# Kernel tuning notes

Hardware: AMD Instinct MI355X
Metric: run time of the kernel (lower is better)

Reference implementation:

```python
import jax, jax.numpy as jnp
import numpy as np

B, T, D, HS = 32, 2048, 384, 64

def setup_inputs() -> dict:
    key = jax.random.key(0)
    kx, kq, kk, kv = jax.random.split(key, 4)
    x = jax.random.normal(kx, (B, T, D), dtype=jnp.float32)
    s = 1.0 / np.sqrt(D)  # Linear-like init scale
    Wq = jax.random.normal(kq, (D, HS), dtype=jnp.float32) * s
    Wk = jax.random.normal(kk, (D, HS), dtype=jnp.float32) * s
    Wv = jax.random.normal(kv, (D, HS), dtype=jnp.float32) * s
    return {"x": x, "Wq": Wq, "Wk": Wk, "Wv": Wv}

def reference(x, Wq, Wk, Wv):
    # Single-head causal self-attention (dropout in eval mode -> identity).
    Tlen = x.shape[1]
    q = x @ Wq  # [B,T,HS]
    k = x @ Wk
    v = x @ Wv
    scale = q.shape[-1] ** (-0.5)
    wei = jnp.einsum('bqd,bkd->bqk', q, k) * scale  # [B,T,T]
    causal = jnp.tril(jnp.ones((Tlen, Tlen), dtype=bool))
    wei = jnp.where(causal, wei, jnp.finfo(wei.dtype).min)
    wei = jax.nn.softmax(wei, axis=-1)
    return jnp.einsum('bqk,bkd->bqd', wei, v)  # [B,T,HS]
```

## Files before the change

### kernel.cpp

```cpp
#include <hip/hip_runtime.h>
#include <hip/hip_bf16.h>

#define T_LEN 2048
#define NBATCH 32

typedef __bf16 bf16x8 __attribute__((ext_vector_type(8)));
typedef float f32x4 __attribute__((ext_vector_type(4)));

__device__ __forceinline__ unsigned short f2bf(float f) {
  return __builtin_bit_cast(unsigned short, __float2bfloat16(f));
}
__device__ __forceinline__ unsigned int pk2(float a, float b) {
  return (unsigned int)f2bf(a) | ((unsigned int)f2bf(b) << 16);
}
__device__ __forceinline__ bf16x8 ld16(const void* p) {
  return __builtin_bit_cast(bf16x8, *(const uint4*)p);
}
__device__ __forceinline__ void gl_lds16(const void* g, void* l) {
  __builtin_amdgcn_global_load_lds(
      (const __attribute__((address_space(1))) unsigned int*)g,
      (__attribute__((address_space(3))) unsigned int*)l, 16, 0, 0);
}
__device__ __forceinline__ void bar_raw() {
  asm volatile("s_barrier" ::: "memory");
}

__global__ __launch_bounds__(256) void k_wprep(const float* __restrict__ Wq,
                                               const float* __restrict__ Wk,
                                               const float* __restrict__ Wv,
                                               unsigned short* __restrict__ Wt3) {
  int idx = blockIdx.x * 256 + threadIdx.x;
  if (idx >= 192 * 384) return;
  int c = idx / 384;
  int k = idx % 384;
  const float* W = (c < 64) ? Wq : ((c < 128) ? Wk : Wv);
  Wt3[idx] = f2bf(W[k * 64 + (c & 63)]);
}

__global__ __launch_bounds__(256) void k_proj(const float* __restrict__ x,
                                              const unsigned short* __restrict__ Wt3,
                                              unsigned short* __restrict__ Qb,
                                              unsigned short* __restrict__ Kb,
                                              unsigned short* __restrict__ VTb) {
  __shared__ __align__(16) unsigned short xs[128 * 32];
  __shared__ __align__(16) unsigned short wt[192 * 32];
  const int tid = threadIdx.x;
  const int lane = tid & 63, w = tid >> 6;
  const int g = lane >> 4, lr = lane & 15;
  const long row0 = (long)blockIdx.x * 128;

  f32x4 acc[2][12] = {};

  for (int ks = 0; ks < 12; ++ks) {
    const int k0 = ks * 32;
    __syncthreads();
    {
      int r = tid >> 1, c0 = (tid & 1) * 16;
      const float4* src = reinterpret_cast<const float4*>(&x[(row0 + r) * 384 + k0 + c0]);
      float4 f0 = src[0], f1 = src[1], f2 = src[2], f3 = src[3];
      uint4 u0, u1;
      u0.x = pk2(f0.x, f0.y); u0.y = pk2(f0.z, f0.w);
      u0.z = pk2(f1.x, f1.y); u0.w = pk2(f1.z, f1.w);
      u1.x = pk2(f2.x, f2.y); u1.y = pk2(f2.z, f2.w);
      u1.z = pk2(f3.x, f3.y); u1.w = pk2(f3.z, f3.w);
      int b0 = (r * 64 + c0 * 2) ^ ((r & 7) << 4);
      int b1 = (r * 64 + c0 * 2 + 16) ^ ((r & 7) << 4);
      *reinterpret_cast<uint4*>((char*)xs + b0) = u0;
      *reinterpret_cast<uint4*>((char*)xs + b1) = u1;
    }
#pragma unroll
    for (int j = 0; j < 3; ++j) {
      int chunk = tid + 256 * j;
      int r = chunk >> 2, c8 = chunk & 3;
      uint4 d = *reinterpret_cast<const uint4*>(&Wt3[r * 384 + k0 + c8 * 8]);
      int b = (r * 64 + c8 * 16) ^ ((r & 7) << 4);
      *reinterpret_cast<uint4*>((char*)wt + b) = d;
    }
    __syncthreads();

    bf16x8 a[2];
#pragma unroll
    for (int mt = 0; mt < 2; ++mt) {
      int r = w * 32 + mt * 16 + lr;
      a[mt] = ld16((char*)xs + ((r * 64 + g * 16) ^ ((r & 7) << 4)));
    }
#pragma unroll
    for (int n = 0; n < 12; ++n) {
      int r = n * 16 + lr;
      bf16x8 bb = ld16((char*)wt + ((r * 64 + g * 16) ^ ((r & 7) << 4)));
      acc[0][n] = __builtin_amdgcn_mfma_f32_16x16x32_bf16(a[0], bb, acc[0][n], 0, 0, 0);
      acc[1][n] = __builtin_amdgcn_mfma_f32_16x16x32_bf16(a[1], bb, acc[1][n], 0, 0, 0);
    }
  }

#pragma unroll
  for (int mt = 0; mt < 2; ++mt)
#pragma unroll
    for (int n = 0; n < 12; ++n)
#pragma unroll
      for (int rr = 0; rr < 4; ++rr) {
        long grow = row0 + w * 32 + mt * 16 + g * 4 + rr;
        int col = n * 16 + lr;
        unsigned short hv = f2bf(acc[mt][n][rr]);
        if (n < 4) {
          Qb[grow * 64 + col] = hv;
        } else if (n < 8) {
          Kb[grow * 64 + (col - 64)] = hv;
        } else {
          long bb_ = grow >> 11;
          long t = grow & 2047;
          VTb[(bb_ * 64 + (col - 128)) * 2048 + t] = hv;
        }
      }
}

__global__ __launch_bounds__(256, 4) void k_attn(const unsigned short* __restrict__ Qb,
                                                 const unsigned short* __restrict__ Kb,
                                                 const unsigned short* __restrict__ VTb,
                                                 float* __restrict__ out) {
  __shared__ __align__(16) char ksm[2 * 8192];
  __shared__ __align__(16) char vsm[2 * 8192];
  __shared__ __align__(16) unsigned short psm[4 * 16 * 64];

  const int tid = threadIdx.x;
  const int lane = tid & 63, w = tid >> 6;
  const int g = lane >> 4, lr = lane & 15;
  const int b = blockIdx.x;
  const int p = blockIdx.y;

  const char* Kg = (const char*)(Kb + (long)b * T_LEN * 64);
  const char* Vg = (const char*)(VTb + (long)b * 64 * 2048);

  const int lrow = lane >> 3;
  const int lsw = (((lane & 7) ^ lrow) << 4);

  const float C2 = 0.125f * 1.44269504f;
  char* pbase = (char*)psm + w * 2048;

  for (int phase = 0; phase < 2; ++phase) {
    const int qt = phase ? p : (31 - p);
    const int qrow0 = qt * 64 + w * 16;
    const int nkv = qt + 1;

    bf16x8 qf[2];
#pragma unroll
    for (int c = 0; c < 2; ++c)
      qf[c] = ld16(&Qb[((long)(b * T_LEN + qrow0 + lr)) * 64 + c * 32 + g * 8]);

    f32x4 o[4] = {};
    float m2[4], l_r[4];
#pragma unroll
    for (int r = 0; r < 4; ++r) { m2[r] = -1e30f; l_r[r] = 0.f; }

    {
      const char* gk = Kg + ((long)(w * 16 + lrow)) * 128 + lsw;
      const char* gv = Vg + ((long)(w * 16 + lrow)) * 4096 + lsw;
      char* kb = ksm + w * 2048;
      char* vb = vsm + w * 2048;
      gl_lds16(gk, kb);             gl_lds16(gk + 8 * 128, kb + 1024);
      gl_lds16(gv, vb);             gl_lds16(gv + 8 * 4096, vb + 1024);
    }

    int cur = 0;
    for (int t = 0; t < nkv; ++t) {
      const int kv0 = t * 64;

      bar_raw();

      if (t + 1 < nkv) {
        const int kv1 = kv0 + 64;
        const char* gk = Kg + ((long)(kv1 + w * 16 + lrow)) * 128 + lsw;
        const char* gv = Vg + ((long)(w * 16 + lrow)) * 4096 + (long)kv1 * 2 + lsw;
        char* kb = ksm + (cur ^ 1) * 8192 + w * 2048;
        char* vb = vsm + (cur ^ 1) * 8192 + w * 2048;
        gl_lds16(gk, kb);           gl_lds16(gk + 8 * 128, kb + 1024);
        gl_lds16(gv, vb);           gl_lds16(gv + 8 * 4096, vb + 1024);
        asm volatile("s_waitcnt vmcnt(4)" ::: "memory");
      } else {
        asm volatile("s_waitcnt vmcnt(0)" ::: "memory");
      }
      bar_raw();

      char* kt = ksm + cur * 8192;
      char* vt = vsm + cur * 8192;

      f32x4 s[4] = {};
      __builtin_amdgcn_s_setprio(1);
#pragma unroll
      for (int c = 0; c < 2; ++c)
#pragma unroll
        for (int n = 0; n < 4; ++n) {
          int r = n * 16 + lr;
          bf16x8 kf = ld16(kt + ((r * 128 + c * 64 + g * 16) ^ ((r & 7) << 4)));
          s[n] = __builtin_amdgcn_mfma_f32_16x16x32_bf16(qf[c], kf, s[n], 0, 0, 0);
        }
      __builtin_amdgcn_s_setprio(0);

      if (t == qt) {
#pragma unroll
        for (int n = 0; n < 4; ++n)
#pragma unroll
          for (int r = 0; r < 4; ++r) {
            int col = kv0 + n * 16 + lr;
            int rowq = qrow0 + g * 4 + r;
            if (col > rowq) s[n][r] = -1e30f;
          }
      }

      float pm[4];
#pragma unroll
      for (int r = 0; r < 4; ++r)
        pm[r] = fmaxf(fmaxf(s[0][r], s[1][r]), fmaxf(s[2][r], s[3][r]));
      bool need = false;
#pragma unroll
      for (int r = 0; r < 4; ++r) need = need || (pm[r] * C2 > m2[r] + 11.5f);
      if (__any((int)need)) {
#pragma unroll
        for (int r = 0; r < 4; ++r) {
          float mx = pm[r];
          mx = fmaxf(mx, __shfl_xor(mx, 1));
          mx = fmaxf(mx, __shfl_xor(mx, 2));
          mx = fmaxf(mx, __shfl_xor(mx, 4));
          mx = fmaxf(mx, __shfl_xor(mx, 8));
          float mn = fmaxf(m2[r], mx * C2);
          float sc = exp2f(m2[r] - mn);
          m2[r] = mn;
          l_r[r] *= sc;
#pragma unroll
          for (int n = 0; n < 4; ++n) o[n][r] *= sc;
        }
      }
      float pr[4][4];
#pragma unroll
      for (int r = 0; r < 4; ++r)
#pragma unroll
        for (int n = 0; n < 4; ++n) {
          float pv = exp2f(__builtin_fmaf(s[n][r], C2, -m2[r]));
          pr[n][r] = pv;
          l_r[r] += pv;
        }

#pragma unroll
      for (int n = 0; n < 4; ++n)
#pragma unroll
        for (int r = 0; r < 4; ++r) {
          int rq = g * 4 + r;
          int col = n * 16 + lr;
          *(unsigned short*)(pbase + ((rq * 128 + col * 2) ^ ((rq & 7) << 4))) = f2bf(pr[n][r]);
        }

      bf16x8 pf[2];
#pragma unroll
      for (int c = 0; c < 2; ++c)
        pf[c] = ld16(pbase + ((lr * 128 + c * 64 + g * 16) ^ ((lr & 7) << 4)));
      __builtin_amdgcn_s_setprio(1);
#pragma unroll
      for (int c = 0; c < 2; ++c)
#pragma unroll
        for (int n = 0; n < 4; ++n) {
          int r = n * 16 + lr;
          bf16x8 vf = ld16(vt + ((r * 128 + c * 64 + g * 16) ^ ((r & 7) << 4)));
          o[n] = __builtin_amdgcn_mfma_f32_16x16x32_bf16(pf[c], vf, o[n], 0, 0, 0);
        }
      __builtin_amdgcn_s_setprio(0);

      cur ^= 1;
    }

#pragma unroll
    for (int r = 0; r < 4; ++r) {
      float l = l_r[r];
      l += __shfl_xor(l, 1);
      l += __shfl_xor(l, 2);
      l += __shfl_xor(l, 4);
      l += __shfl_xor(l, 8);
      float inv = 1.0f / l;
#pragma unroll
      for (int n = 0; n < 4; ++n) {
        long rowg = (long)b * T_LEN + qrow0 + g * 4 + r;
        out[rowg * 64 + n * 16 + lr] = o[n][r] * inv;
      }
    }

    bar_raw();
  }
}

extern "C" void kernel_launch(void* const* d_in, const int* in_sizes, int n_in,
                              void* d_out, int out_size, void* d_ws, size_t ws_size,
                              hipStream_t stream) {
  const float* x  = (const float*)d_in[0];
  const float* Wq = (const float*)d_in[1];
  const float* Wk = (const float*)d_in[2];
  const float* Wv = (const float*)d_in[3];
  float* out = (float*)d_out;

  char* ws = (char*)d_ws;
  unsigned short* Wt3 = (unsigned short*)ws;
  unsigned short* Qb  = (unsigned short*)(ws + 0x80000);
  unsigned short* Kb  = (unsigned short*)(ws + 0x80000 + 0x800000);
  unsigned short* VTb = (unsigned short*)(ws + 0x80000 + 0x1000000);

  k_wprep<<<dim3(288), dim3(256), 0, stream>>>(Wq, Wk, Wv, Wt3);
  k_proj<<<dim3(512), dim3(256), 0, stream>>>(x, Wt3, Qb, Kb, VTb);
  k_attn<<<dim3(NBATCH, 16), dim3(256), 0, stream>>>(Qb, Kb, VTb, out);
}
```

Before: 90.28 us.

## Use one query tile per block with 32-wide KV tiles and higher occupancy

Drops the paired long/short query-tile scheme and launches one block per 64-row query tile (grid 32x32), in heaviest-first order. KV tiles shrink from 64 to 32 keys, which halves LDS per block and raises launch bounds to 8 waves per SIMD. Each wave also skips KV tiles that lie entirely above its own causal diagonal. The trade-off is that causal load balancing now depends on the hardware scheduler, and there are twice as many loop iterations and barriers per unit of work.

```diff
diff --git a/kernel.cpp b/kernel.cpp
--- a/kernel.cpp
+++ b/kernel.cpp
@@ -114,91 +114,83 @@
       }
 }
 
-__global__ __launch_bounds__(256, 4) void k_attn(const unsigned short* __restrict__ Qb,
+__global__ __launch_bounds__(256, 8) void k_attn(const unsigned short* __restrict__ Qb,
                                                  const unsigned short* __restrict__ Kb,
                                                  const unsigned short* __restrict__ VTb,
                                                  float* __restrict__ out) {
-  __shared__ __align__(16) char ksm[2 * 8192];
-  __shared__ __align__(16) char vsm[2 * 8192];
-  __shared__ __align__(16) unsigned short psm[4 * 16 * 64];
+  __shared__ __align__(16) char ksm[2 * 4096];
+  __shared__ __align__(16) char vsm[2 * 4096];
+  __shared__ __align__(16) char psm[4 * 1024];
 
   const int tid = threadIdx.x;
   const int lane = tid & 63, w = tid >> 6;
   const int g = lane >> 4, lr = lane & 15;
   const int b = blockIdx.x;
-  const int p = blockIdx.y;
+  const int qt = (gridDim.y - 1) - blockIdx.y;
+  const int qrow0 = qt * 64 + w * 16;
 
   const char* Kg = (const char*)(Kb + (long)b * T_LEN * 64);
   const char* Vg = (const char*)(VTb + (long)b * 64 * 2048);
 
-  const int lrow = lane >> 3;
-  const int lsw = (((lane & 7) ^ lrow) << 4);
+  const int lrowK = lane >> 3;
+  const int lswK = (((lane & 7) ^ lrowK) << 4);
+  const int vrow = lane >> 2;
+  const int vcol = (lane & 3) << 4;
+
+  bf16x8 qf[2];
+#pragma unroll
+  for (int c = 0; c < 2; ++c)
+    qf[c] = ld16(&Qb[((long)(b * T_LEN + qrow0 + lr)) * 64 + c * 32 + g * 8]);
+
+  f32x4 o[4] = {};
+  float m2[4], l_r[4];
+#pragma unroll
+  for (int r = 0; r < 4; ++r) { m2[r] = -1e30f; l_r[r] = 0.f; }
 
   const float C2 = 0.125f * 1.44269504f;
-  char* pbase = (char*)psm + w * 2048;
-
-  for (int phase = 0; phase < 2; ++phase) {
-    const int qt = phase ? p : (31 - p);
-    const int qrow0 = qt * 64 + w * 16;
-    const int nkv = qt + 1;
-
-    bf16x8 qf[2];
-#pragma unroll
-    for (int c = 0; c < 2; ++c)
-      qf[c] = ld16(&Qb[((long)(b * T_LEN + qrow0 + lr)) * 64 + c * 32 + g * 8]);
-
-    f32x4 o[4] = {};
-    float m2[4], l_r[4];
-#pragma unroll
-    for (int r = 0; r < 4; ++r) { m2[r] = -1e30f; l_r[r] = 0.f; }
-
-    {
-      const char* gk = Kg + ((long)(w * 16 + lrow)) * 128 + lsw;
-      const char* gv = Vg + ((long)(w * 16 + lrow)) * 4096 + lsw;
-      char* kb = ksm + w * 2048;
-      char* vb = vsm + w * 2048;
-      gl_lds16(gk, kb);             gl_lds16(gk + 8 * 128, kb + 1024);
-      gl_lds16(gv, vb);             gl_lds16(gv + 8 * 4096, vb + 1024);
-    }
-
-    int cur = 0;
-    for (int t = 0; t < nkv; ++t) {
-      const int kv0 = t * 64;
-
-      bar_raw();
-
-      if (t + 1 < nkv) {
-        const int kv1 = kv0 + 64;
-        const char* gk = Kg + ((long)(kv1 + w * 16 + lrow)) * 128 + lsw;
-        const char* gv = Vg + ((long)(w * 16 + lrow)) * 4096 + (long)kv1 * 2 + lsw;
-        char* kb = ksm + (cur ^ 1) * 8192 + w * 2048;
-        char* vb = vsm + (cur ^ 1) * 8192 + w * 2048;
-        gl_lds16(gk, kb);           gl_lds16(gk + 8 * 128, kb + 1024);
-        gl_lds16(gv, vb);           gl_lds16(gv + 8 * 4096, vb + 1024);
-        asm volatile("s_waitcnt vmcnt(4)" ::: "memory");
-      } else {
-        asm volatile("s_waitcnt vmcnt(0)" ::: "memory");
-      }
-      bar_raw();
-
-      char* kt = ksm + cur * 8192;
-      char* vt = vsm + cur * 8192;
-
-      f32x4 s[4] = {};
+  char* pbase = psm + w * 1024;
+  const int nkv = 2 * qt + 2;
+
+  gl_lds16(Kg + (long)(w * 8 + lrowK) * 128 + lswK, ksm + w * 1024);
+  gl_lds16(Vg + (long)(w * 16 + vrow) * 4096 + vcol, vsm + w * 1024);
+
+  int cur = 0;
+  for (int t = 0; t < nkv; ++t) {
+    const int kv0 = t * 32;
+
+    bar_raw();
+
+    if (t + 1 < nkv) {
+      const int kv1 = kv0 + 32;
+      gl_lds16(Kg + (long)(kv1 + w * 8 + lrowK) * 128 + lswK,
+               ksm + (cur ^ 1) * 4096 + w * 1024);
+      gl_lds16(Vg + (long)(w * 16 + vrow) * 4096 + (long)kv1 * 2 + vcol,
+               vsm + (cur ^ 1) * 4096 + w * 1024);
+      asm volatile("s_waitcnt vmcnt(2)" ::: "memory");
+    } else {
+      asm volatile("s_waitcnt vmcnt(0)" ::: "memory");
+    }
+    bar_raw();
+
+    if (kv0 <= qrow0 + 15) {
+      char* kt = ksm + cur * 4096;
+      char* vt = vsm + cur * 4096;
+
+      f32x4 s[2] = {};
       __builtin_amdgcn_s_setprio(1);
 #pragma unroll
       for (int c = 0; c < 2; ++c)
 #pragma unroll
-        for (int n = 0; n < 4; ++n) {
+        for (int n = 0; n < 2; ++n) {
           int r = n * 16 + lr;
           bf16x8 kf = ld16(kt + ((r * 128 + c * 64 + g * 16) ^ ((r & 7) << 4)));
           s[n] = __builtin_amdgcn_mfma_f32_16x16x32_bf16(qf[c], kf, s[n], 0, 0, 0);
         }
       __builtin_amdgcn_s_setprio(0);
 
-      if (t == qt) {
-#pragma unroll
-        for (int n = 0; n < 4; ++n)
+      if (kv0 + 31 > qrow0) {
+#pragma unroll
+        for (int n = 0; n < 2; ++n)
 #pragma unroll
           for (int r = 0; r < 4; ++r) {
             int col = kv0 + n * 16 + lr;
@@ -209,8 +201,7 @@
 
       float pm[4];
 #pragma unroll
-      for (int r = 0; r < 4; ++r)
-        pm[r] = fmaxf(fmaxf(s[0][r], s[1][r]), fmaxf(s[2][r], s[3][r]));
+      for (int r = 0; r < 4; ++r) pm[r] = fmaxf(s[0][r], s[1][r]);
       bool need = false;
 #pragma unroll
       for (int r = 0; r < 4; ++r) need = need || (pm[r] * C2 > m2[r] + 11.5f);
@@ -230,59 +221,51 @@
           for (int n = 0; n < 4; ++n) o[n][r] *= sc;
         }
       }
-      float pr[4][4];
-#pragma unroll
-      for (int r = 0; r < 4; ++r)
-#pragma unroll
-        for (int n = 0; n < 4; ++n) {
+#pragma unroll
+      for (int n = 0; n < 2; ++n)
+#pragma unroll
+        for (int r = 0; r < 4; ++r) {
           float pv = exp2f(__builtin_fmaf(s[n][r], C2, -m2[r]));
-          pr[n][r] = pv;
+          s[n][r] = pv;
           l_r[r] += pv;
         }
 
 #pragma unroll
-      for (int n = 0; n < 4; ++n)
+      for (int n = 0; n < 2; ++n)
 #pragma unroll
         for (int r = 0; r < 4; ++r) {
           int rq = g * 4 + r;
           int col = n * 16 + lr;
-          *(unsigned short*)(pbase + ((rq * 128 + col * 2) ^ ((rq & 7) << 4))) = f2bf(pr[n][r]);
-        }
-
-      bf16x8 pf[2];
-#pragma unroll
-      for (int c = 0; c < 2; ++c)
-        pf[c] = ld16(pbase + ((lr * 128 + c * 64 + g * 16) ^ ((lr & 7) << 4)));
+          *(unsigned short*)(pbase + rq * 64 + ((col * 2) ^ (g << 4))) = f2bf(s[n][r]);
+        }
+
+      bf16x8 pf = ld16(pbase + lr * 64 + ((g * 16) ^ ((lr >> 2) << 4)));
       __builtin_amdgcn_s_setprio(1);
 #pragma unroll
-      for (int c = 0; c < 2; ++c)
-#pragma unroll
-        for (int n = 0; n < 4; ++n) {
-          int r = n * 16 + lr;
-          bf16x8 vf = ld16(vt + ((r * 128 + c * 64 + g * 16) ^ ((r & 7) << 4)));
-          o[n] = __builtin_amdgcn_mfma_f32_16x16x32_bf16(pf[c], vf, o[n], 0, 0, 0);
-        }
+      for (int n = 0; n < 4; ++n) {
+        int rd = n * 16 + lr;
+        bf16x8 vf = ld16(vt + rd * 64 + g * 16);
+        o[n] = __builtin_amdgcn_mfma_f32_16x16x32_bf16(pf, vf, o[n], 0, 0, 0);
+      }
       __builtin_amdgcn_s_setprio(0);
-
-      cur ^= 1;
-    }
-
-#pragma unroll
-    for (int r = 0; r < 4; ++r) {
-      float l = l_r[r];
-      l += __shfl_xor(l, 1);
-      l += __shfl_xor(l, 2);
-      l += __shfl_xor(l, 4);
-      l += __shfl_xor(l, 8);
-      float inv = 1.0f / l;
-#pragma unroll
-      for (int n = 0; n < 4; ++n) {
-        long rowg = (long)b * T_LEN + qrow0 + g * 4 + r;
-        out[rowg * 64 + n * 16 + lr] = o[n][r] * inv;
-      }
-    }
-
-    bar_raw();
+    }
+
+    cur ^= 1;
+  }
+
+#pragma unroll
+  for (int r = 0; r < 4; ++r) {
+    float l = l_r[r];
+    l += __shfl_xor(l, 1);
+    l += __shfl_xor(l, 2);
+    l += __shfl_xor(l, 4);
+    l += __shfl_xor(l, 8);
+    float inv = 1.0f / l;
+#pragma unroll
+    for (int n = 0; n < 4; ++n) {
+      long rowg = (long)b * T_LEN + qrow0 + g * 4 + r;
+      out[rowg * 64 + n * 16 + lr] = o[n][r] * inv;
+    }
   }
 }
 
@@ -303,5 +286,5 @@
 
   k_wprep<<<dim3(288), dim3(256), 0, stream>>>(Wq, Wk, Wv, Wt3);
   k_proj<<<dim3(512), dim3(256), 0, stream>>>(x, Wt3, Qb, Kb, VTb);
-  k_attn<<<dim3(NBATCH, 16), dim3(256), 0, stream>>>(Qb, Kb, VTb, out);
-}
+  k_attn<<<dim3(NBATCH, 32), dim3(256), 0, stream>>>(Qb, Kb, VTb, out);
+}
```

After: 124.1 us. 1.37x slower.

## Use 512-thread blocks over 128-row query tiles, dropping paired-tile phase loop

Applied to the files above, without the earlier changes.

The attention kernel moves from 256-thread blocks that each process two 64-row query tiles (paired for load balance) to 512-thread blocks with eight waves covering one 128-row query tile. Each K/V tile loaded into LDS is now shared by twice as many waves, and each wave issues one load per tile instead of two. Waves whose rows lie entirely before a KV tile skip its compute. The bf16 conversion of P switches to plain truncation. In exchange, blocks with larger query indices run longer, causing imbalance, and occupancy changes with the larger blocks.

```diff
diff --git a/kernel.cpp b/kernel.cpp
--- a/kernel.cpp
+++ b/kernel.cpp
@@ -12,6 +12,9 @@
 }
 __device__ __forceinline__ unsigned int pk2(float a, float b) {
   return (unsigned int)f2bf(a) | ((unsigned int)f2bf(b) << 16);
+}
+__device__ __forceinline__ unsigned int f2bf_tr(float f) {
+  return __builtin_bit_cast(unsigned int, f) >> 16;
 }
 __device__ __forceinline__ bf16x8 ld16(const void* p) {
   return __builtin_bit_cast(bf16x8, *(const uint4*)p);
@@ -114,19 +117,20 @@
       }
 }
 
-__global__ __launch_bounds__(256, 4) void k_attn(const unsigned short* __restrict__ Qb,
-                                                 const unsigned short* __restrict__ Kb,
-                                                 const unsigned short* __restrict__ VTb,
-                                                 float* __restrict__ out) {
+__global__ __launch_bounds__(512) void k_attn(const unsigned short* __restrict__ Qb,
+                                              const unsigned short* __restrict__ Kb,
+                                              const unsigned short* __restrict__ VTb,
+                                              float* __restrict__ out) {
   __shared__ __align__(16) char ksm[2 * 8192];
   __shared__ __align__(16) char vsm[2 * 8192];
-  __shared__ __align__(16) unsigned short psm[4 * 16 * 64];
+  __shared__ __align__(16) char psm[8 * 2048];
 
   const int tid = threadIdx.x;
   const int lane = tid & 63, w = tid >> 6;
   const int g = lane >> 4, lr = lane & 15;
   const int b = blockIdx.x;
-  const int p = blockIdx.y;
+  const int qt = (gridDim.y - 1) - blockIdx.y;
+  const int qrow0 = qt * 128 + w * 16;
 
   const char* Kg = (const char*)(Kb + (long)b * T_LEN * 64);
   const char* Vg = (const char*)(VTb + (long)b * 64 * 2048);
@@ -134,53 +138,42 @@
   const int lrow = lane >> 3;
   const int lsw = (((lane & 7) ^ lrow) << 4);
 
+  bf16x8 qf[2];
+#pragma unroll
+  for (int c = 0; c < 2; ++c)
+    qf[c] = ld16(&Qb[((long)(b * T_LEN + qrow0 + lr)) * 64 + c * 32 + g * 8]);
+
+  f32x4 o[4] = {};
+  float m2[4], l_r[4];
+#pragma unroll
+  for (int r = 0; r < 4; ++r) { m2[r] = -1e30f; l_r[r] = 0.f; }
+
   const float C2 = 0.125f * 1.44269504f;
-  char* pbase = (char*)psm + w * 2048;
-
-  for (int phase = 0; phase < 2; ++phase) {
-    const int qt = phase ? p : (31 - p);
-    const int qrow0 = qt * 64 + w * 16;
-    const int nkv = qt + 1;
-
-    bf16x8 qf[2];
-#pragma unroll
-    for (int c = 0; c < 2; ++c)
-      qf[c] = ld16(&Qb[((long)(b * T_LEN + qrow0 + lr)) * 64 + c * 32 + g * 8]);
-
-    f32x4 o[4] = {};
-    float m2[4], l_r[4];
-#pragma unroll
-    for (int r = 0; r < 4; ++r) { m2[r] = -1e30f; l_r[r] = 0.f; }
-
-    {
-      const char* gk = Kg + ((long)(w * 16 + lrow)) * 128 + lsw;
-      const char* gv = Vg + ((long)(w * 16 + lrow)) * 4096 + lsw;
-      char* kb = ksm + w * 2048;
-      char* vb = vsm + w * 2048;
-      gl_lds16(gk, kb);             gl_lds16(gk + 8 * 128, kb + 1024);
-      gl_lds16(gv, vb);             gl_lds16(gv + 8 * 4096, vb + 1024);
-    }
-
-    int cur = 0;
-    for (int t = 0; t < nkv; ++t) {
-      const int kv0 = t * 64;
-
-      bar_raw();
-
-      if (t + 1 < nkv) {
-        const int kv1 = kv0 + 64;
-        const char* gk = Kg + ((long)(kv1 + w * 16 + lrow)) * 128 + lsw;
-        const char* gv = Vg + ((long)(w * 16 + lrow)) * 4096 + (long)kv1 * 2 + lsw;
-        char* kb = ksm + (cur ^ 1) * 8192 + w * 2048;
-        char* vb = vsm + (cur ^ 1) * 8192 + w * 2048;
-        gl_lds16(gk, kb);           gl_lds16(gk + 8 * 128, kb + 1024);
-        gl_lds16(gv, vb);           gl_lds16(gv + 8 * 4096, vb + 1024);
-        asm volatile("s_waitcnt vmcnt(4)" ::: "memory");
-      } else {
-        asm volatile("s_waitcnt vmcnt(0)" ::: "memory");
-      }
-      bar_raw();
-
+  char* pbase = psm + w * 2048;
+  const int nkv = 2 * qt + 2;
+
+  gl_lds16(Kg + (long)(w * 8 + lrow) * 128 + lsw, ksm + w * 1024);
+  gl_lds16(Vg + (long)(w * 8 + lrow) * 4096 + lsw, vsm + w * 1024);
+
+  int cur = 0;
+  for (int t = 0; t < nkv; ++t) {
+    const int kv0 = t * 64;
+
+    bar_raw();
+
+    if (t + 1 < nkv) {
+      const int kv1 = kv0 + 64;
+      gl_lds16(Kg + (long)(kv1 + w * 8 + lrow) * 128 + lsw,
+               ksm + (cur ^ 1) * 8192 + w * 1024);
+      gl_lds16(Vg + (long)(w * 8 + lrow) * 4096 + (long)kv1 * 2 + lsw,
+               vsm + (cur ^ 1) * 8192 + w * 1024);
+      asm volatile("s_waitcnt vmcnt(2)" ::: "memory");
+    } else {
+      asm volatile("s_waitcnt vmcnt(0)" ::: "memory");
+    }
+    bar_raw();
+
+    if (kv0 <= qrow0 + 15) {
       char* kt = ksm + cur * 8192;
       char* vt = vsm + cur * 8192;
 
@@ -196,7 +189,7 @@
         }
       __builtin_amdgcn_s_setprio(0);
 
-      if (t == qt) {
+      if (kv0 + 63 > qrow0) {
 #pragma unroll
         for (int n = 0; n < 4; ++n)
 #pragma unroll
@@ -246,7 +239,8 @@
         for (int r = 0; r < 4; ++r) {
           int rq = g * 4 + r;
           int col = n * 16 + lr;
-          *(unsigned short*)(pbase + ((rq * 128 + col * 2) ^ ((rq & 7) << 4))) = f2bf(pr[n][r]);
+          *(unsigned short*)(pbase + ((rq * 128 + col * 2) ^ ((rq & 7) << 4))) =
+              (unsigned short)f2bf_tr(pr[n][r]);
         }
 
       bf16x8 pf[2];
@@ -263,26 +257,24 @@
           o[n] = __builtin_amdgcn_mfma_f32_16x16x32_bf16(pf[c], vf, o[n], 0, 0, 0);
         }
       __builtin_amdgcn_s_setprio(0);
-
-      cur ^= 1;
-    }
-
-#pragma unroll
-    for (int r = 0; r < 4; ++r) {
-      float l = l_r[r];
-      l += __shfl_xor(l, 1);
-      l += __shfl_xor(l, 2);
-      l += __shfl_xor(l, 4);
-      l += __shfl_xor(l, 8);
-      float inv = 1.0f / l;
-#pragma unroll
-      for (int n = 0; n < 4; ++n) {
-        long rowg = (long)b * T_LEN + qrow0 + g * 4 + r;
-        out[rowg * 64 + n * 16 + lr] = o[n][r] * inv;
-      }
-    }
-
-    bar_raw();
+    }
+
+    cur ^= 1;
+  }
+
+#pragma unroll
+  for (int r = 0; r < 4; ++r) {
+    float l = l_r[r];
+    l += __shfl_xor(l, 1);
+    l += __shfl_xor(l, 2);
+    l += __shfl_xor(l, 4);
+    l += __shfl_xor(l, 8);
+    float inv = 1.0f / l;
+#pragma unroll
+    for (int n = 0; n < 4; ++n) {
+      long rowg = (long)b * T_LEN + qrow0 + g * 4 + r;
+      out[rowg * 64 + n * 16 + lr] = o[n][r] * inv;
+    }
   }
 }
 
@@ -303,5 +295,5 @@
 
   k_wprep<<<dim3(288), dim3(256), 0, stream>>>(Wq, Wk, Wv, Wt3);
   k_proj<<<dim3(512), dim3(256), 0, stream>>>(x, Wt3, Qb, Kb, VTb);
-  k_attn<<<dim3(NBATCH, 16), dim3(256), 0, stream>>>(Qb, Kb, VTb, out);
-}
+  k_attn<<<dim3(NBATCH, 16), dim3(512), 0, stream>>>(Qb, Kb, VTb, out);
+}
```

New measurement: 90.68 us. No clear change (+0.4%).
